# Kernel tuning notes

Hardware: AMD Instinct MI355X
Metric: run time of the kernel (lower is better)

## Reference

```python
import jax, jax.numpy as jnp
import numpy as np

B, I, T, H, O = 256, 128, 256, 512, 2
EPS = 1e-5  # BatchNorm1d default eps


def setup_inputs() -> dict:
    key = jax.random.key(0)
    ks = jax.random.split(key, 32)
    stdv = 1.0 / np.sqrt(H)
    u = lambda k, shape: jax.random.uniform(k, shape, jnp.float32, -stdv, stdv)
    X = jax.random.normal(ks[0], (B, I, T), jnp.float32)
    Mask = (jax.random.uniform(ks[1], (B, I, T)) > 0.5).astype(jnp.float32)
    Delta = jax.random.uniform(ks[2], (B, I, T)) * 5.0
    inp = jnp.stack([X, Mask, Delta], axis=1)  # [B, 3, I, T]
    return dict(
        input=inp,
        x_mean=jnp.float32(0.0),
        W_dg_x=u(ks[3], (I, I)), b_dg_x=u(ks[4], (I,)),
        W_dg_h=u(ks[5], (I, H)), b_dg_h=u(ks[6], (H,)),
        W_xz=u(ks[7], (I, H)), W_hz=u(ks[8], (H, H)), W_mz=u(ks[9], (I, H)), b_z=u(ks[10], (H,)),
        W_xr=u(ks[11], (I, H)), W_hr=u(ks[12], (H, H)), W_mr=u(ks[13], (I, H)), b_r=u(ks[14], (H,)),
        W_xh=u(ks[15], (I, H)), W_hh=u(ks[16], (H, H)), W_mh=u(ks[17], (I, H)), b_h=u(ks[18], (H,)),
        W_hy=u(ks[19], (H, O)), b_hy=u(ks[20], (O,)),
        bn_gamma=u(ks[21], (H,)), bn_beta=u(ks[22], (H,)),
    )


def reference(input, x_mean, W_dg_x, b_dg_x, W_dg_h, b_dg_h,
              W_xz, W_hz, W_mz, b_z, W_xr, W_hr, W_mr, b_r,
              W_xh, W_hh, W_mh, b_h, W_hy, b_hy, bn_gamma, bn_beta):
    # input: [B, 3, I, T] -> time-major [T, B, I]
    Xs = jnp.transpose(input[:, 0], (2, 0, 1))
    Ms = jnp.transpose(input[:, 1], (2, 0, 1))
    Ds = jnp.transpose(input[:, 2], (2, 0, 1))
    b, i = input.shape[0], input.shape[2]
    h0 = jnp.zeros((b, W_hz.shape[0]), input.dtype)       # Hidden_State buffer (zeros, broadcast over batch)
    xl0 = jnp.zeros((b, i), input.dtype)                   # X_last_obs buffer

    def step(carry, xs):
        h, x_last = carry
        x, m, d = xs
        gamma_x = jnp.exp(-jax.nn.relu(d @ W_dg_x + b_dg_x))   # [B, I]
        gamma_h = jnp.exp(-jax.nn.relu(d @ W_dg_h + b_dg_h))   # [B, H]
        x_last = jnp.where(m > 0, x, x_last)
        x = m * x + (1 - m) * (gamma_x * x_last + (1 - gamma_x) * x_mean)
        h = gamma_h * h
        z = jax.nn.sigmoid(x @ W_xz + h @ W_hz + m @ W_mz + b_z)
        r = jax.nn.sigmoid(x @ W_xr + h @ W_hr + m @ W_mr + b_r)
        h_tilde = jnp.tanh(x @ W_xh + (r * h) @ W_hh + m @ W_mh + b_h)
        h = (1 - z) * h + z * h_tilde
        # BatchNorm1d in training mode: batch mean, biased variance
        mu = h.mean(axis=0)
        var = ((h - mu) ** 2).mean(axis=0)
        h = bn_gamma * (h - mu) * jax.lax.rsqrt(var + EPS) + bn_beta
        y = jax.nn.softplus(h @ W_hy + b_hy)
        return (h, x_last), (y, h)

    _, (ys, hs) = jax.lax.scan(step, (h0, xl0), (Xs, Ms, Ds))
    # back to batch-major [B, T, *]
    return jnp.transpose(ys, (1, 0, 2)), jnp.transpose(hs, (1, 0, 2))
```

## Files before the change

### kernel.cpp

```cpp
#include <hip/hip_runtime.h>
#include <math.h>

#define Bb 256
#define Ii 128
#define Tt 256
#define Hh 512
#define Oo 2
#define TBr (Tt*Bb)
#define EPS_BN 1e-5f

typedef __attribute__((ext_vector_type(8))) short short8;
typedef __attribute__((ext_vector_type(8))) __bf16 bf16x8;
typedef __attribute__((ext_vector_type(4))) float f32x4;
typedef unsigned long long u64;

__device__ __forceinline__ f32x4 mfma_bf16(short8 a, short8 b, f32x4 c) {
    return __builtin_amdgcn_mfma_f32_16x16x32_bf16(
        __builtin_bit_cast(bf16x8, a), __builtin_bit_cast(bf16x8, b), c, 0, 0, 0);
}
__device__ __forceinline__ short f2bf(float f) {
    union { float f; unsigned u; } v; v.f = f;
    unsigned r = (v.u + 0x7FFFu + ((v.u >> 16) & 1u)) >> 16;
    return (short)r;
}
__device__ __forceinline__ float bf2f(short s) {
    union { unsigned u; float f; } v; v.u = ((unsigned)(unsigned short)s) << 16;
    return v.f;
}
__device__ __forceinline__ float sigmoidf_(float x) { return 1.f / (1.f + expf(-x)); }
__device__ __forceinline__ float softplusf_(float x) { return fmaxf(x, 0.f) + log1pf(expf(-fabsf(x))); }

#define ALD_F(p)  __hip_atomic_load((p),  __ATOMIC_RELAXED, __HIP_MEMORY_SCOPE_AGENT)
#define AST_F(p,v) __hip_atomic_store((p), (v), __ATOMIC_RELAXED, __HIP_MEMORY_SCOPE_AGENT)
#define AADD_F(p,v) (void)__hip_atomic_fetch_add((p), (v), __ATOMIC_RELAXED, __HIP_MEMORY_SCOPE_AGENT)

__device__ __forceinline__ short8 ald16(const short* p) {
    union { u64 u[2]; short8 s; } v;
    v.u[0] = ALD_F((const u64*)p);
    v.u[1] = ALD_F((const u64*)(p + 4));
    return v.s;
}
__device__ __forceinline__ u64 pack4bf(float a, float b, float c_, float d) {
    return (u64)(unsigned short)f2bf(a)
         | ((u64)(unsigned short)f2bf(b) << 16)
         | ((u64)(unsigned short)f2bf(c_) << 32)
         | ((u64)(unsigned short)f2bf(d) << 48);
}

__global__ __launch_bounds__(1024) void repack_kernel(const float* __restrict__ in,
                                                      float* __restrict__ Xall,
                                                      short* __restrict__ Mall,
                                                      short* __restrict__ Dall)
{
    __shared__ float tile[32][33];
    const int bz = blockIdx.z;
    const int b = bz / 3, cch = bz % 3;
    const int t0 = blockIdx.x * 32, i0 = blockIdx.y * 32;
    const int tx = threadIdx.x, ty = threadIdx.y;
    const float* src = in + ((size_t)b * 3 + cch) * (size_t)Ii * Tt;
    tile[ty][tx] = src[(size_t)(i0 + ty) * Tt + t0 + tx];
    __syncthreads();
    const float v = tile[tx][ty];
    const size_t off = ((size_t)(t0 + ty) * Bb + b) * Ii + i0 + tx;
    if (cch == 0)      Xall[off] = v;
    else if (cch == 1) Mall[off] = f2bf(v);
    else               Dall[off] = f2bf(v);
}

__global__ __launch_bounds__(256) void pack_weights_kernel(
    const float* __restrict__ W_dg_x, const float* __restrict__ W_dg_h,
    const float* __restrict__ W_xz, const float* __restrict__ W_hz, const float* __restrict__ W_mz, const float* __restrict__ b_z,
    const float* __restrict__ W_xr, const float* __restrict__ W_hr, const float* __restrict__ W_mr, const float* __restrict__ b_r,
    const float* __restrict__ W_xh, const float* __restrict__ W_hh, const float* __restrict__ W_mh,
    short* __restrict__ Wc1T, short* __restrict__ Wc2T,
    short* __restrict__ WdgxT, short* __restrict__ WdghT, float* __restrict__ bias1)
{
    const int idx = blockIdx.x * blockDim.x + threadIdx.x;
    const int n1 = 1024 * 768, n2 = 512 * 768, n3 = 128 * 128, n4 = 512 * 128;
    if (idx < n1) {
        const int n = idx / 768, k = idx % 768;
        const int col = (n < Hh) ? n : (n - Hh);
        const float* Wx = (n < Hh) ? W_xz : W_xr;
        const float* Wm = (n < Hh) ? W_mz : W_mr;
        const float* Wh = (n < Hh) ? W_hz : W_hr;
        float v;
        if (k < Ii)        v = Wx[(size_t)k * Hh + col];
        else if (k < 2*Ii) v = Wm[(size_t)(k - Ii) * Hh + col];
        else               v = Wh[(size_t)(k - 2*Ii) * Hh + col];
        Wc1T[idx] = f2bf(v);
    } else if (idx < n1 + n2) {
        const int j = idx - n1;
        const int n = j / 768, k = j % 768;
        float v;
        if (k < Ii)        v = W_xh[(size_t)k * Hh + n];
        else if (k < 2*Ii) v = W_mh[(size_t)(k - Ii) * Hh + n];
        else               v = W_hh[(size_t)(k - 2*Ii) * Hh + n];
        Wc2T[j] = f2bf(v);
    } else if (idx < n1 + n2 + n3) {
        const int j = idx - n1 - n2;
        const int n = j >> 7, k = j & 127;
        WdgxT[j] = f2bf(W_dg_x[(size_t)k * Ii + n]);
    } else if (idx < n1 + n2 + n3 + n4) {
        const int j = idx - n1 - n2 - n3;
        const int n = j >> 7, k = j & 127;
        WdghT[j] = f2bf(W_dg_h[(size_t)k * Hh + n]);
    } else if (idx < n1 + n2 + n3 + n4 + 1024) {
        const int n = idx - n1 - n2 - n3 - n4;
        bias1[n] = (n < Hh) ? b_z[n] : b_r[n - Hh];
    }
}

__global__ __launch_bounds__(64) void gdecay_kernel(const short* __restrict__ A,
                                                    const short* __restrict__ BT,
                                                    const float* __restrict__ bias,
                                                    short* __restrict__ C, int N)
{
    const int lane = threadIdx.x;
    const int c = lane & 15, g = lane >> 4;
    const int m0 = blockIdx.x * 32, n0 = blockIdx.y * 64;
    const short* a0 = A + (size_t)(m0 + c) * Ii + 8 * g;
    const short* a1 = a0 + (size_t)16 * Ii;
    const short* bw = BT + (size_t)(n0 + c) * Ii + 8 * g;
    f32x4 acc[2][4];
    #pragma unroll
    for (int i = 0; i < 2; ++i)
        #pragma unroll
        for (int f = 0; f < 4; ++f) acc[i][f] = (f32x4){0.f, 0.f, 0.f, 0.f};
    #pragma unroll
    for (int k0 = 0; k0 < 128; k0 += 32) {
        const short8 av0 = *(const short8*)(a0 + k0);
        const short8 av1 = *(const short8*)(a1 + k0);
        #pragma unroll
        for (int fn = 0; fn < 4; ++fn) {
            const short8 bv = *(const short8*)(bw + (size_t)fn * 16 * Ii + k0);
            acc[0][fn] = mfma_bf16(av0, bv, acc[0][fn]);
            acc[1][fn] = mfma_bf16(av1, bv, acc[1][fn]);
        }
    }
    #pragma unroll
    for (int fn = 0; fn < 4; ++fn) {
        const int n = n0 + fn * 16 + c;
        const float bs = bias[n];
        #pragma unroll
        for (int fm = 0; fm < 2; ++fm) {
            #pragma unroll
            for (int j = 0; j < 4; ++j) {
                const int m = m0 + fm * 16 + 4 * g + j;
                const float v = expf(-fmaxf(acc[fm][fn][j] + bs, 0.f));
                C[(size_t)m * N + n] = f2bf(v);
            }
        }
    }
}

__global__ __launch_bounds__(256) void xeff_scan_kernel(const float* __restrict__ Xall,
                                                        const short* __restrict__ Mall,
                                                        const short* __restrict__ Gx,
                                                        const float* __restrict__ xmean_p,
                                                        short* __restrict__ Xe)
{
    const int bi = blockIdx.x * blockDim.x + threadIdx.x;
    if (bi >= Bb * Ii) return;
    const float xm = xmean_p[0];
    float xl = 0.f;
    for (int t = 0; t < Tt; ++t) {
        const size_t off = (size_t)t * Bb * Ii + bi;
        const float x = Xall[off];
        const float m = bf2f(Mall[off]);
        const float gx = bf2f(Gx[off]);
        if (m > 0.f) xl = x;
        Xe[off] = f2bf(m * x + (1.f - m) * (gx * xl + (1.f - gx) * xm));
    }
}

#define XM_STR 264
#define HP_STR 520
#define GH_STR 520

__global__ __launch_bounds__(512, 1) void grud_persistent(
    const short* __restrict__ Xe, const short* __restrict__ Ma,
    const short* __restrict__ Ghb,
    const short* __restrict__ Wc1T, const short* __restrict__ Wc2T,
    const float* __restrict__ bias1, const float* __restrict__ b_h,
    const float* __restrict__ bn_g, const float* __restrict__ bn_b,
    const float* __restrict__ Why, const float* __restrict__ bhy,
    short* __restrict__ rhG,
    short* __restrict__ HrawG,
    float* __restrict__ PstSum,
    int* __restrict__ f1,
    int* __restrict__ f2,
    float* __restrict__ out_hs, float* __restrict__ out_ys)
{
    const int bid = blockIdx.x, tid = threadIdx.x;
    const int w = tid >> 6, lane = tid & 63, c = lane & 15, g = lane >> 4;
    const int mt = bid & 15, ng = bid >> 4;
    const int m0 = mt * 16;

    __shared__ short sXM[16 * XM_STR];
    __shared__ short sHP[16 * HP_STR];
    __shared__ short sGH[16 * GH_STR];
    __shared__ float sZ[32 * 17];
    __shared__ float scratch[1536];
    __shared__ float sWhy[1024];
    __shared__ float scs[512], shs[512];
    __shared__ float ysred[16];

    sWhy[tid] = Why[tid]; sWhy[tid + 512] = Why[tid + 512];
    const float bhy0 = bhy[0], bhy1 = bhy[1];

    const int colt = w & 3, kh = w >> 2;
    const int colbaseA = (colt < 2) ? (ng * 32 + colt * 16)
                                    : (512 + ng * 32 + (colt - 2) * 16);
    short8 wA[12];
    {
        const short* bw = Wc1T + (size_t)(colbaseA + c) * 768 + kh * 384 + 8 * g;
        #pragma unroll
        for (int s = 0; s < 12; ++s) wA[s] = *(const short8*)(bw + 32 * s);
    }
    const int colt2 = w & 1, kq = w >> 1;
    const int colbaseB = ng * 32 + colt2 * 16;
    short8 wB[6];
    {
        const short* bw = Wc2T + (size_t)(colbaseB + c) * 768 + kq * 192 + 8 * g;
        #pragma unroll
        for (int s = 0; s < 6; ++s) wB[s] = *(const short8*)(bw + 32 * s);
    }
    const int npeer = (kq == 1) ? 4 : (kq >= 2 ? 6 : 0);
    const int peer0 = (kq == 1) ? 0 : (kq == 2 ? 4 : 10);
    const int peerflag = (lane < npeer) ? ((mt + 16 * (peer0 + lane)) * 16) : -1;

    {
        const int r = tid >> 5, cu = tid & 31;
        const short* src = (cu < 16)
            ? (Xe + ((size_t)(m0 + r)) * Ii + 8 * cu)
            : (Ma + ((size_t)(m0 + r)) * Ii + 8 * (cu - 16));
        *(short8*)(&sXM[r * XM_STR + 8 * cu]) = *(const short8*)src;
    }
    __syncthreads();

    for (int t = 0; t < Tt; ++t) {
        f32x4 accA = (f32x4){0.f, 0.f, 0.f, 0.f};
        f32x4 accB = (f32x4){0.f, 0.f, 0.f, 0.f};
        if (kh == 0) {
            #pragma unroll
            for (int s = 0; s < 8; ++s)
                accA = mfma_bf16(wA[s],
                    *(const short8*)(&sXM[c * XM_STR + 32 * s + 8 * g]), accA);
        }
        #pragma unroll
        for (int s = 0; s < 6; ++s) {
            const int k = kq * 192 + 32 * s;
            if (k < 256)
                accB = mfma_bf16(wB[s],
                    *(const short8*)(&sXM[c * XM_STR + k + 8 * g]), accB);
        }

        if (t > 0) {
            const int pR = (t + 2) % 3;
            {
                const float s1 = ALD_F(&PstSum[pR * 1024 + tid]);
                const float s2 = ALD_F(&PstSum[pR * 1024 + 512 + tid]);
                const float mu = s1 * (1.f / 256.f);
                const float var = fmaxf(s2 * (1.f / 256.f) - mu * mu, 0.f);
                const float sc = bn_g[tid] * rsqrtf(var + EPS_BN);
                scs[tid] = sc; shs[tid] = bn_b[tid] - mu * sc;
            }
            __syncthreads();
            float p0 = 0.f, p1 = 0.f;
            #pragma unroll
            for (int i = 0; i < 4; ++i) {
                const int idx = tid + i * 512;
                const int r = idx >> 7, c4 = (idx & 127) * 4;
                union { u64 u; unsigned short us[4]; } hv, gv;
                hv.u = ALD_F((const u64*)(HrawG + (size_t)(m0 + r) * Hh + c4));
                gv.u = *(const u64*)(&sGH[r * GH_STR + c4]);
                float h[4];
                #pragma unroll
                for (int j = 0; j < 4; ++j)
                    h[j] = fmaf(bf2f((short)hv.us[j]), scs[c4 + j], shs[c4 + j]);
                *(u64*)(&sHP[r * HP_STR + c4]) =
                    pack4bf(h[0] * bf2f((short)gv.us[0]), h[1] * bf2f((short)gv.us[1]),
                            h[2] * bf2f((short)gv.us[2]), h[3] * bf2f((short)gv.us[3]));
                if ((c4 >> 5) == ng) {
                    *(f32x4*)(&out_hs[((size_t)(m0 + r) * Tt + (t - 1)) * Hh + c4]) =
                        (f32x4){h[0], h[1], h[2], h[3]};
                }
                if (r == ng) {
                    #pragma unroll
                    for (int j = 0; j < 4; ++j) {
                        p0 = fmaf(h[j], sWhy[2 * (c4 + j)], p0);
                        p1 = fmaf(h[j], sWhy[2 * (c4 + j) + 1], p1);
                    }
                }
            }
            #pragma unroll
            for (int s = 1; s < 64; s <<= 1) { p0 += __shfl_xor(p0, s); p1 += __shfl_xor(p1, s); }
            if (lane == 0) { ysred[2 * w] = p0; ysred[2 * w + 1] = p1; }
            __syncthreads();
            if (tid == 0) {
                float q0 = 0.f, q1 = 0.f;
                #pragma unroll
                for (int i = 0; i < 8; ++i) { q0 += ysred[2 * i]; q1 += ysred[2 * i + 1]; }
                out_ys[((size_t)(m0 + ng) * Tt + (t - 1)) * Oo + 0] = softplusf_(q0 + bhy0);
                out_ys[((size_t)(m0 + ng) * Tt + (t - 1)) * Oo + 1] = softplusf_(q1 + bhy1);
            }
        } else {
            #pragma unroll
            for (int i = 0; i < 4; ++i) {
                const int idx = tid + i * 512;
                const int r = idx >> 7, c4 = (idx & 127) * 4;
                *(u64*)(&sHP[r * HP_STR + c4]) = 0ull;
            }
            __syncthreads();
        }

        if (kh == 0) {
            #pragma unroll
            for (int s = 8; s < 12; ++s)
                accA = mfma_bf16(wA[s],
                    *(const short8*)(&sHP[c * HP_STR + (32 * s - 256) + 8 * g]), accA);
        } else {
            #pragma unroll
            for (int s = 0; s < 12; ++s)
                accA = mfma_bf16(wA[s],
                    *(const short8*)(&sHP[c * HP_STR + 128 + 32 * s + 8 * g]), accA);
        }
        if (kh == 1) {
            float* sp = scratch + (colt * 64 + lane) * 4;
            sp[0] = accA[0]; sp[1] = accA[1]; sp[2] = accA[2]; sp[3] = accA[3];
        }
        __syncthreads();
        if (kh == 0) {
            const float* sp = scratch + (colt * 64 + lane) * 4;
            accA[0] += sp[0]; accA[1] += sp[1]; accA[2] += sp[2]; accA[3] += sp[3];
            if (colt < 2) {
                #pragma unroll
                for (int j = 0; j < 4; ++j) {
                    const int lc = colt * 16 + 4 * g + j;
                    const float v = sigmoidf_(accA[j] + bias1[ng * 32 + lc]);
                    sZ[lc * 17 + c] = v;
                }
            } else {
                const int nn0 = ng * 32 + (colt - 2) * 16 + 4 * g;
                float rv[4];
                #pragma unroll
                for (int j = 0; j < 4; ++j) {
                    const float v = sigmoidf_(accA[j] + bias1[512 + nn0 + j]);
                    rv[j] = v * bf2f(sHP[c * HP_STR + nn0 + j]);
                }
                AST_F((u64*)(rhG + ((size_t)(m0 + c) * Hh + nn0)),
                      pack4bf(rv[0], rv[1], rv[2], rv[3]));
            }
        }
        __syncthreads();
        if (tid == 0) AST_F(&f1[bid * 16], t + 1);
        if (t + 1 < Tt) {
            #pragma unroll
            for (int i = 0; i < 4; ++i) {
                const int idx = tid + i * 512;
                const int r = idx >> 7, c4 = (idx & 127) * 4;
                const u64 v = *(const u64*)(Ghb + ((size_t)(t + 1) * Bb + m0 + r) * Hh + c4);
                *(u64*)(&sGH[r * GH_STR + c4]) = v;
            }
        }
        if (tid < 4) AST_F(&PstSum[((t + 1) % 3) * 1024 + bid * 4 + tid], 0.f);

        if (npeer > 0) {
            for (;;) {
                const int v = (lane < npeer)
                    ? __hip_atomic_load(&f1[peerflag], __ATOMIC_RELAXED, __HIP_MEMORY_SCOPE_AGENT)
                    : 0x7fffffff;
                if (__all(v >= t + 1)) break;
                __builtin_amdgcn_s_sleep(1);
            }
            asm volatile("" ::: "memory");
        }
        #pragma unroll
        for (int s = 0; s < 6; ++s) {
            const int k = kq * 192 + 32 * s;
            if (k >= 256)
                accB = mfma_bf16(wB[s],
                    ald16(rhG + (size_t)(m0 + c) * Hh + (k - 256) + 8 * g), accB);
        }
        if (kq > 0) {
            float* sp = scratch + ((colt2 * 3 + kq - 1) * 64 + lane) * 4;
            sp[0] = accB[0]; sp[1] = accB[1]; sp[2] = accB[2]; sp[3] = accB[3];
        }
        __syncthreads();
        if (kq == 0) {
            #pragma unroll
            for (int qq = 0; qq < 3; ++qq) {
                const float* sp = scratch + ((colt2 * 3 + qq) * 64 + lane) * 4;
                accB[0] += sp[0]; accB[1] += sp[1]; accB[2] += sp[2]; accB[3] += sp[3];
            }
            const int pC = t % 3;
            float hr4[4];
            #pragma unroll
            for (int j = 0; j < 4; ++j) {
                const int lc = colt2 * 16 + 4 * g + j;
                const int col = ng * 32 + lc;
                const float pre = accB[j] + b_h[col];
                const float z = sZ[lc * 17 + c];
                const float hp = bf2f(sHP[c * HP_STR + col]);
                const float hr = (1.f - z) * hp + z * tanhf(pre);
                hr4[j] = hr;
                float sp_ = hr, sq_ = hr * hr;
                sp_ += __shfl_xor(sp_, 1); sq_ += __shfl_xor(sq_, 1);
                sp_ += __shfl_xor(sp_, 2); sq_ += __shfl_xor(sq_, 2);
                sp_ += __shfl_xor(sp_, 4); sq_ += __shfl_xor(sq_, 4);
                sp_ += __shfl_xor(sp_, 8); sq_ += __shfl_xor(sq_, 8);
                if (c == 0) {
                    AADD_F(&PstSum[pC * 1024 + col], sp_);
                    AADD_F(&PstSum[pC * 1024 + 512 + col], sq_);
                }
            }
            const int cb = ng * 32 + colt2 * 16 + 4 * g;
            AST_F((u64*)(HrawG + (size_t)(m0 + c) * Hh + cb),
                  pack4bf(hr4[0], hr4[1], hr4[2], hr4[3]));
        }
        __syncthreads();
        if (tid == 0) AST_F(&f2[bid * 16], t + 1);
        if (t + 1 < Tt) {
            const int r = tid >> 5, cu = tid & 31;
            const short* src = (cu < 16)
                ? (Xe + ((size_t)(t + 1) * Bb + m0 + r) * Ii + 8 * cu)
                : (Ma + ((size_t)(t + 1) * Bb + m0 + r) * Ii + 8 * (cu - 16));
            *(short8*)(&sXM[r * XM_STR + 8 * cu]) = *(const short8*)src;
        }
        if (tid < 64) {
            for (;;) {
                const int v0 = __hip_atomic_load(&f2[(tid * 4 + 0) * 16], __ATOMIC_RELAXED, __HIP_MEMORY_SCOPE_AGENT);
                const int v1 = __hip_atomic_load(&f2[(tid * 4 + 1) * 16], __ATOMIC_RELAXED, __HIP_MEMORY_SCOPE_AGENT);
                const int v2 = __hip_atomic_load(&f2[(tid * 4 + 2) * 16], __ATOMIC_RELAXED, __HIP_MEMORY_SCOPE_AGENT);
                const int v3 = __hip_atomic_load(&f2[(tid * 4 + 3) * 16], __ATOMIC_RELAXED, __HIP_MEMORY_SCOPE_AGENT);
                int mn = v0 < v1 ? v0 : v1;
                mn = mn < v2 ? mn : v2;
                mn = mn < v3 ? mn : v3;
                if (__all(mn >= t + 1)) break;
                __builtin_amdgcn_s_sleep(1);
            }
        }
        __syncthreads();
    }

    {
        const int pR = (Tt - 1) % 3;
        {
            const float s1 = ALD_F(&PstSum[pR * 1024 + tid]);
            const float s2 = ALD_F(&PstSum[pR * 1024 + 512 + tid]);
            const float mu = s1 * (1.f / 256.f);
            const float var = fmaxf(s2 * (1.f / 256.f) - mu * mu, 0.f);
            const float sc = bn_g[tid] * rsqrtf(var + EPS_BN);
            scs[tid] = sc; shs[tid] = bn_b[tid] - mu * sc;
        }
        __syncthreads();
        float p0 = 0.f, p1 = 0.f;
        #pragma unroll
        for (int i = 0; i < 4; ++i) {
            const int idx = tid + i * 512;
            const int r = idx >> 7, c4 = (idx & 127) * 4;
            union { u64 u; unsigned short us[4]; } hv;
            hv.u = ALD_F((const u64*)(HrawG + (size_t)(m0 + r) * Hh + c4));
            float h[4];
            #pragma unroll
            for (int j = 0; j < 4; ++j)
                h[j] = fmaf(bf2f((short)hv.us[j]), scs[c4 + j], shs[c4 + j]);
            if ((c4 >> 5) == ng) {
                *(f32x4*)(&out_hs[((size_t)(m0 + r) * Tt + (Tt - 1)) * Hh + c4]) =
                    (f32x4){h[0], h[1], h[2], h[3]};
            }
            if (r == ng) {
                #pragma unroll
                for (int j = 0; j < 4; ++j) {
                    p0 = fmaf(h[j], sWhy[2 * (c4 + j)], p0);
                    p1 = fmaf(h[j], sWhy[2 * (c4 + j) + 1], p1);
                }
            }
        }
        #pragma unroll
        for (int s = 1; s < 64; s <<= 1) { p0 += __shfl_xor(p0, s); p1 += __shfl_xor(p1, s); }
        if (lane == 0) { ysred[2 * w] = p0; ysred[2 * w + 1] = p1; }
        __syncthreads();
        if (tid == 0) {
            float q0 = 0.f, q1 = 0.f;
            #pragma unroll
            for (int i = 0; i < 8; ++i) { q0 += ysred[2 * i]; q1 += ysred[2 * i + 1]; }
            out_ys[((size_t)(m0 + ng) * Tt + (Tt - 1)) * Oo + 0] = softplusf_(q0 + bhy0);
            out_ys[((size_t)(m0 + ng) * Tt + (Tt - 1)) * Oo + 1] = softplusf_(q1 + bhy1);
        }
    }
}

extern "C" void kernel_launch(void* const* d_in, const int* in_sizes, int n_in,
                              void* d_out, int out_size, void* d_ws, size_t ws_size,
                              hipStream_t stream)
{
    const float* input  = (const float*)d_in[0];
    const float* xmean  = (const float*)d_in[1];
    const float* W_dg_x = (const float*)d_in[2];
    const float* b_dg_x = (const float*)d_in[3];
    const float* W_dg_h = (const float*)d_in[4];
    const float* b_dg_h = (const float*)d_in[5];
    const float* W_xz   = (const float*)d_in[6];
    const float* W_hz   = (const float*)d_in[7];
    const float* W_mz   = (const float*)d_in[8];
    const float* b_z    = (const float*)d_in[9];
    const float* W_xr   = (const float*)d_in[10];
    const float* W_hr   = (const float*)d_in[11];
    const float* W_mr   = (const float*)d_in[12];
    const float* b_r    = (const float*)d_in[13];
    const float* W_xh   = (const float*)d_in[14];
    const float* W_hh   = (const float*)d_in[15];
    const float* W_mh   = (const float*)d_in[16];
    const float* b_h    = (const float*)d_in[17];
    const float* W_hy   = (const float*)d_in[18];
    const float* b_hy   = (const float*)d_in[19];
    const float* bn_g   = (const float*)d_in[20];
    const float* bn_b   = (const float*)d_in[21];

    float* out_ys = (float*)d_out;
    float* out_hs = out_ys + (size_t)Bb * Tt * Oo;

    char* p = (char*)d_ws;
    float* Xall = (float*)p;            p += (size_t)TBr * Ii * 4;
    short* Mall = (short*)p;            p += (size_t)TBr * Ii * 2;
    short* Dall = (short*)p;            p += (size_t)TBr * Ii * 2;
    short* Gxb  = (short*)p;            p += (size_t)TBr * Ii * 2;
    short* Ghb  = (short*)p;            p += (size_t)TBr * Hh * 2;
    short* Xe   = (short*)p;            p += (size_t)TBr * Ii * 2;
    short* Wc1T = (short*)p;            p += (size_t)1024 * 768 * 2;
    short* Wc2T = (short*)p;            p += (size_t)512 * 768 * 2;
    short* WdgxT= (short*)p;            p += (size_t)128 * 128 * 2;
    short* WdghT= (short*)p;            p += (size_t)512 * 128 * 2;
    float* bias1= (float*)p;            p += 1024 * 4;
    short* rhG  = (short*)p;            p += (size_t)Bb * Hh * 2;
    short* HrawG= (short*)p;            p += (size_t)Bb * Hh * 2;
    float* PstSum=(float*)p;            p += 3 * 1024 * 4;
    int*   f1   = (int*)p;              p += 256 * 16 * 4;
    int*   f2   = (int*)p;              p += 256 * 16 * 4;

    hipMemsetAsync(f1, 0, 256 * 16 * 4, stream);
    hipMemsetAsync(f2, 0, 256 * 16 * 4, stream);
    hipMemsetAsync(PstSum, 0, 3 * 1024 * 4, stream);

    repack_kernel<<<dim3(Tt / 32, Ii / 32, Bb * 3), dim3(32, 32), 0, stream>>>(input, Xall, Mall, Dall);

    {
        const int total = 1024 * 768 + 512 * 768 + 128 * 128 + 512 * 128 + 1024;
        pack_weights_kernel<<<(total + 255) / 256, 256, 0, stream>>>(
            W_dg_x, W_dg_h,
            W_xz, W_hz, W_mz, b_z,
            W_xr, W_hr, W_mr, b_r,
            W_xh, W_hh, W_mh,
            Wc1T, Wc2T, WdgxT, WdghT, bias1);
    }

    gdecay_kernel<<<dim3(TBr / 32, Ii / 64), 64, 0, stream>>>(Dall, WdgxT, b_dg_x, Gxb, Ii);
    gdecay_kernel<<<dim3(TBr / 32, Hh / 64), 64, 0, stream>>>(Dall, WdghT, b_dg_h, Ghb, Hh);

    xeff_scan_kernel<<<(Bb * Ii) / 256, 256, 0, stream>>>(Xall, Mall, Gxb, xmean, Xe);

    grud_persistent<<<256, 512, 0, stream>>>(
        Xe, Mall, Ghb, Wc1T, Wc2T, bias1, b_h, bn_g, bn_b,
        W_hy, b_hy, rhG, HrawG, PstSum, f1, f2, out_hs, out_ys);
}
```

Measured before the change: 2.721 ms.

## Move output head and hs stores off the recurrent critical path

The hs output store and the W_hy projection with its softplus are moved out of the BN-apply phase. They now run after the f1 flag is published, so this work fills the time spent waiting for peer blocks. The H loads are hoisted before the PstSum loads so the two latencies overlap, and the HrawG store is issued before the shuffle reductions and atomic adds. The cost is 16 extra registers to hold normalized h values and an added __syncthreads per step.

After: 2.294 ms. 15.7% less time.

```diff
diff --git a/kernel.cpp b/kernel.cpp
--- a/kernel.cpp
+++ b/kernel.cpp
@@ -238,6 +238,8 @@
     }
     __syncthreads();
 
+    float hkeep[16];
+
     for (int t = 0; t < Tt; ++t) {
         f32x4 accA = (f32x4){0.f, 0.f, 0.f, 0.f};
         f32x4 accB = (f32x4){0.f, 0.f, 0.f, 0.f};
@@ -257,53 +259,40 @@
 
         if (t > 0) {
             const int pR = (t + 2) % 3;
+            u64 hvu[4];
+            #pragma unroll
+            for (int i = 0; i < 4; ++i) {
+                const int idx = tid + i * 512;
+                const int r = idx >> 7, c4 = (idx & 127) * 4;
+                hvu[i] = ALD_F((const u64*)(HrawG + (size_t)(m0 + r) * Hh + c4));
+            }
+            const float s1 = ALD_F(&PstSum[pR * 1024 + tid]);
+            const float s2 = ALD_F(&PstSum[pR * 1024 + 512 + tid]);
             {
-                const float s1 = ALD_F(&PstSum[pR * 1024 + tid]);
-                const float s2 = ALD_F(&PstSum[pR * 1024 + 512 + tid]);
                 const float mu = s1 * (1.f / 256.f);
                 const float var = fmaxf(s2 * (1.f / 256.f) - mu * mu, 0.f);
                 const float sc = bn_g[tid] * rsqrtf(var + EPS_BN);
                 scs[tid] = sc; shs[tid] = bn_b[tid] - mu * sc;
             }
             __syncthreads();
-            float p0 = 0.f, p1 = 0.f;
             #pragma unroll
             for (int i = 0; i < 4; ++i) {
                 const int idx = tid + i * 512;
                 const int r = idx >> 7, c4 = (idx & 127) * 4;
                 union { u64 u; unsigned short us[4]; } hv, gv;
-                hv.u = ALD_F((const u64*)(HrawG + (size_t)(m0 + r) * Hh + c4));
+                hv.u = hvu[i];
                 gv.u = *(const u64*)(&sGH[r * GH_STR + c4]);
                 float h[4];
                 #pragma unroll
-                for (int j = 0; j < 4; ++j)
+                for (int j = 0; j < 4; ++j) {
                     h[j] = fmaf(bf2f((short)hv.us[j]), scs[c4 + j], shs[c4 + j]);
+                    hkeep[i * 4 + j] = h[j];
+                }
                 *(u64*)(&sHP[r * HP_STR + c4]) =
                     pack4bf(h[0] * bf2f((short)gv.us[0]), h[1] * bf2f((short)gv.us[1]),
                             h[2] * bf2f((short)gv.us[2]), h[3] * bf2f((short)gv.us[3]));
-                if ((c4 >> 5) == ng) {
-                    *(f32x4*)(&out_hs[((size_t)(m0 + r) * Tt + (t - 1)) * Hh + c4]) =
-                        (f32x4){h[0], h[1], h[2], h[3]};
-                }
-                if (r == ng) {
-                    #pragma unroll
-                    for (int j = 0; j < 4; ++j) {
-                        p0 = fmaf(h[j], sWhy[2 * (c4 + j)], p0);
-                        p1 = fmaf(h[j], sWhy[2 * (c4 + j) + 1], p1);
-                    }
-                }
-            }
-            #pragma unroll
-            for (int s = 1; s < 64; s <<= 1) { p0 += __shfl_xor(p0, s); p1 += __shfl_xor(p1, s); }
-            if (lane == 0) { ysred[2 * w] = p0; ysred[2 * w + 1] = p1; }
+            }
             __syncthreads();
-            if (tid == 0) {
-                float q0 = 0.f, q1 = 0.f;
-                #pragma unroll
-                for (int i = 0; i < 8; ++i) { q0 += ysred[2 * i]; q1 += ysred[2 * i + 1]; }
-                out_ys[((size_t)(m0 + ng) * Tt + (t - 1)) * Oo + 0] = softplusf_(q0 + bhy0);
-                out_ys[((size_t)(m0 + ng) * Tt + (t - 1)) * Oo + 1] = softplusf_(q1 + bhy1);
-            }
         } else {
             #pragma unroll
             for (int i = 0; i < 4; ++i) {
@@ -354,6 +343,28 @@
         }
         __syncthreads();
         if (tid == 0) AST_F(&f1[bid * 16], t + 1);
+        if (t > 0) {
+            float p0 = 0.f, p1 = 0.f;
+            #pragma unroll
+            for (int i = 0; i < 4; ++i) {
+                const int idx = tid + i * 512;
+                const int r = idx >> 7, c4 = (idx & 127) * 4;
+                if ((c4 >> 5) == ng) {
+                    *(f32x4*)(&out_hs[((size_t)(m0 + r) * Tt + (t - 1)) * Hh + c4]) =
+                        (f32x4){hkeep[i*4+0], hkeep[i*4+1], hkeep[i*4+2], hkeep[i*4+3]};
+                }
+                if (r == ng) {
+                    #pragma unroll
+                    for (int j = 0; j < 4; ++j) {
+                        p0 = fmaf(hkeep[i*4+j], sWhy[2 * (c4 + j)], p0);
+                        p1 = fmaf(hkeep[i*4+j], sWhy[2 * (c4 + j) + 1], p1);
+                    }
+                }
+            }
+            #pragma unroll
+            for (int s = 1; s < 64; s <<= 1) { p0 += __shfl_xor(p0, s); p1 += __shfl_xor(p1, s); }
+            if (lane == 0) { ysred[2 * w] = p0; ysred[2 * w + 1] = p1; }
+        }
         if (t + 1 < Tt) {
             #pragma unroll
             for (int i = 0; i < 4; ++i) {
@@ -364,6 +375,16 @@
             }
         }
         if (tid < 4) AST_F(&PstSum[((t + 1) % 3) * 1024 + bid * 4 + tid], 0.f);
+        if (t > 0) {
+            __syncthreads();
+            if (tid == 0) {
+                float q0 = 0.f, q1 = 0.f;
+                #pragma unroll
+                for (int i = 0; i < 8; ++i) { q0 += ysred[2 * i]; q1 += ysred[2 * i + 1]; }
+                out_ys[((size_t)(m0 + ng) * Tt + (t - 1)) * Oo + 0] = softplusf_(q0 + bhy0);
+                out_ys[((size_t)(m0 + ng) * Tt + (t - 1)) * Oo + 1] = softplusf_(q1 + bhy1);
+            }
+        }
 
         if (npeer > 0) {
             for (;;) {
@@ -402,21 +423,24 @@
                 const float pre = accB[j] + b_h[col];
                 const float z = sZ[lc * 17 + c];
                 const float hp = bf2f(sHP[c * HP_STR + col]);
-                const float hr = (1.f - z) * hp + z * tanhf(pre);
-                hr4[j] = hr;
-                float sp_ = hr, sq_ = hr * hr;
+                hr4[j] = (1.f - z) * hp + z * tanhf(pre);
+            }
+            const int cb = ng * 32 + colt2 * 16 + 4 * g;
+            AST_F((u64*)(HrawG + (size_t)(m0 + c) * Hh + cb),
+                  pack4bf(hr4[0], hr4[1], hr4[2], hr4[3]));
+            #pragma unroll
+            for (int j = 0; j < 4; ++j) {
+                float sp_ = hr4[j], sq_ = hr4[j] * hr4[j];
                 sp_ += __shfl_xor(sp_, 1); sq_ += __shfl_xor(sq_, 1);
                 sp_ += __shfl_xor(sp_, 2); sq_ += __shfl_xor(sq_, 2);
                 sp_ += __shfl_xor(sp_, 4); sq_ += __shfl_xor(sq_, 4);
                 sp_ += __shfl_xor(sp_, 8); sq_ += __shfl_xor(sq_, 8);
                 if (c == 0) {
+                    const int col = ng * 32 + colt2 * 16 + 4 * g + j;
                     AADD_F(&PstSum[pC * 1024 + col], sp_);
                     AADD_F(&PstSum[pC * 1024 + 512 + col], sq_);
                 }
             }
-            const int cb = ng * 32 + colt2 * 16 + 4 * g;
-            AST_F((u64*)(HrawG + (size_t)(m0 + c) * Hh + cb),
-                  pack4bf(hr4[0], hr4[1], hr4[2], hr4[3]));
         }
         __syncthreads();
         if (tid == 0) AST_F(&f2[bid * 16], t + 1);
```
